# Performance work log

Measured on AMD Instinct MI355X. Metric: run time of the kernel, lower is better.

## Reference

```python
import jax, jax.numpy as jnp
import numpy as np
from math import sqrt

ALPHA = 1.0
EPS = 1e-8


def setup_inputs() -> dict:
    key = jax.random.key(0)
    k1, k2, k3 = jax.random.split(key, 3)
    B, L, S, H, E = 4, 2048, 2048, 8, 64
    queries = jax.random.normal(k1, (B, L, H, E), dtype=jnp.float32)
    keys = jax.random.normal(k2, (B, S, H, E), dtype=jnp.float32)
    values = jax.random.normal(k3, (B, S, H, E), dtype=jnp.float32)
    return {"queries": queries, "keys": keys, "values": values}


def reference(queries, keys, values):
    B, L, H, E = queries.shape
    scale = 1.0 / sqrt(E)
    # [B,H,L,S] dot-product scores
    dot_product = jnp.einsum('blhe,bshe->bhls', queries, keys)
    # squared norms: [B,H,L,1] and [B,H,1,S]
    queries_norm2 = jnp.sum(queries * queries, axis=-1).transpose(0, 2, 1)[..., None]
    keys_norm2 = jnp.sum(keys * keys, axis=-1).transpose(0, 2, 1)[..., None, :]
    # wedge (exterior product) norm: |q|^2|k|^2 - (q.k)^2, clamped at 0
    wedge_norm2 = jax.nn.relu(queries_norm2 * keys_norm2 - dot_product * dot_product)
    wedge_norm = jnp.sqrt(wedge_norm2 + EPS)
    scores = ((1.0 - ALPHA) * dot_product + ALPHA * wedge_norm) * scale
    A = jax.nn.softmax(scores, axis=-1)  # dropout p=0 (eval)
    V = jnp.einsum('bhls,bshd->blhd', A, values)
    return V, jnp.mean(jnp.abs(scores))
```

## Files before the change

kernel.cpp:

```cpp
#include <hip/hip_runtime.h>
#include <hip/hip_bf16.h>


#define B_ 4
#define L_ 2048
#define S_ 2048
#define H_ 8
#define E_ 64
#define EPS_ 1e-8f
#define SC2_ 0.18033688011112042f
#define LN2_ 0.6931471805599453f
#define ROWSTR (H_ * E_)
#define NOUT ((size_t)B_ * L_ * H_ * E_)

#define K_OFF 0
#define V_OFF 8388608
#define KN_OFF 16777216
#define WS_NEED 17039360

typedef __attribute__((ext_vector_type(8))) short bf16x8;
typedef __attribute__((ext_vector_type(4))) float f32x4;
typedef __attribute__((ext_vector_type(2))) float f32x2;

union bfr8 { bf16x8 v; unsigned u[4]; };

static __device__ __forceinline__ unsigned pk2(float lo, float hi) {
  union { __hip_bfloat162 h2; unsigned u; } cv;
  cv.h2 = __float22bfloat162_rn(float2{lo, hi});
  return cv.u;
}
static __device__ __forceinline__ unsigned cvtpk(float lo, float hi) {
  unsigned r;
  asm("v_cvt_pk_bf16_f32 %0, %1, %2" : "=v"(r) : "v"(lo), "v"(hi));
  return r;
}
static __device__ __forceinline__ float fast_sqrt(float x) {
  float r; asm("v_sqrt_f32 %0, %1" : "=v"(r) : "v"(x)); return r;
}
static __device__ __forceinline__ float fast_exp2(float x) {
  float r; asm("v_exp_f32 %0, %1" : "=v"(r) : "v"(x)); return r;
}
static __device__ __forceinline__ void gload16(const void* g, void* l) {
  __builtin_amdgcn_global_load_lds((const __attribute__((address_space(1))) void*)g,
                                   (__attribute__((address_space(3))) void*)l, 16, 0, 0);
}

__global__ void prep_kv(const float* __restrict__ K, const float* __restrict__ V,
                        short* __restrict__ Kg, short* __restrict__ Vg,
                        float* __restrict__ kn2g, float* __restrict__ out) {
  const int tid = threadIdx.x;
  const int bidx = blockIdx.x;
  if (bidx == 0 && tid == 0) out[NOUT] = 0.f;
  const int st = bidx & 31;
  const int bh = bidx >> 5;
  const int b = bh >> 3, h = bh & 7;
  const size_t src_base = (size_t)b * (L_ * ROWSTR) + (size_t)(st * 64) * ROWSTR + (size_t)h * E_;

  {
    short* dst = Kg + (size_t)bidx * 4096;
    const int s = tid >> 2;
    float part = 0.f;
#pragma unroll
    for (int q = 0; q < 2; ++q) {
      const int ch = (2 * tid + q) & 7;
      const int esrc = (ch ^ (s & 7)) * 8;
      const float* sp = K + src_base + (size_t)s * ROWSTR + esrc;
      const float4 a = *reinterpret_cast<const float4*>(sp);
      const float4 c4 = *reinterpret_cast<const float4*>(sp + 4);
      part += a.x*a.x + a.y*a.y + a.z*a.z + a.w*a.w
            + c4.x*c4.x + c4.y*c4.y + c4.z*c4.z + c4.w*c4.w;
      bfr8 o;
      o.u[0] = pk2(a.x, a.y);  o.u[1] = pk2(a.z, a.w);
      o.u[2] = pk2(c4.x, c4.y); o.u[3] = pk2(c4.z, c4.w);
      *reinterpret_cast<bf16x8*>(dst + s * 64 + ch * 8) = o.v;
    }
    part += __shfl_xor(part, 1);
    part += __shfl_xor(part, 2);
    if ((tid & 3) == 0) kn2g[(size_t)bidx * 64 + s] = part;
  }

  {
    short* dst = Vg + (size_t)bidx * 4096;
    const int e = tid & 63;
    const int sc0 = tid >> 6;
#pragma unroll
    for (int q = 0; q < 2; ++q) {
      const int sc = sc0 + q * 4;
      const float* sp = V + src_base + (size_t)(sc * 8) * ROWSTR + e;
      const float v0 = sp[0];
      const float v1 = sp[1 * ROWSTR];
      const float v2 = sp[2 * ROWSTR];
      const float v3 = sp[3 * ROWSTR];
      const float v4 = sp[4 * ROWSTR];
      const float v5 = sp[5 * ROWSTR];
      const float v6 = sp[6 * ROWSTR];
      const float v7 = sp[7 * ROWSTR];
      bfr8 o;
      o.u[0] = pk2(v0, v1); o.u[1] = pk2(v2, v3);
      o.u[2] = pk2(v4, v5); o.u[3] = pk2(v6, v7);
      *reinterpret_cast<bf16x8*>(dst + e * 64 + ((sc ^ (e & 7)) * 8)) = o.v;
    }
  }
}

__launch_bounds__(256, 4)
__global__ void geom_attn(const float* __restrict__ Q,
                          const short* __restrict__ Kg,
                          const short* __restrict__ Vg,
                          const float* __restrict__ kn2g,
                          float* __restrict__ out) {
  __shared__ __align__(16) short Kl[2][4096];
  __shared__ __align__(16) short Vl[2][4096];
  __shared__ __align__(16) short Plds[4][1024];

  const int tid = threadIdx.x;
  const int lane = tid & 63;
  const int w = tid >> 6;
  const int g = lane >> 4;
  const int c = lane & 15;
  const int cx = c & 7;

  const int vbk = ((blockIdx.x & 7) << 7) + (blockIdx.x >> 3);
  const int qt = vbk & 31;
  const int bh = vbk >> 5;
  const int b = bh >> 3, h = bh & 7;
  const int q0 = qt * 64;

  const size_t qbase = (size_t)b * (L_ * ROWSTR) + (size_t)h * E_;

  bfr8 qa[2];
  float qn2sc;
  {
    const int qrow = q0 + w * 16 + c;
    const float* qp = Q + qbase + (size_t)qrow * ROWSTR;
    float qs = 0.f;
#pragma unroll
    for (int ch = 0; ch < 2; ++ch) {
      const float4 a = *reinterpret_cast<const float4*>(qp + ch * 32 + g * 8);
      const float4 b4 = *reinterpret_cast<const float4*>(qp + ch * 32 + g * 8 + 4);
      qa[ch].u[0] = pk2(a.x, a.y);  qa[ch].u[1] = pk2(a.z, a.w);
      qa[ch].u[2] = pk2(b4.x, b4.y); qa[ch].u[3] = pk2(b4.z, b4.w);
      qs += a.x*a.x + a.y*a.y + a.z*a.z + a.w*a.w
          + b4.x*b4.x + b4.y*b4.y + b4.z*b4.z + b4.w*b4.w;
    }
    qs += __shfl_xor(qs, 16);
    qs += __shfl_xor(qs, 32);
    qn2sc = qs;
  }
  const f32x2 qn2v = {qn2sc, qn2sc};
  const f32x2 eps2 = {EPS_, EPS_};
  const f32x2 sc2v = {SC2_, SC2_};

  f32x2 lsA = {0.f, 0.f}, lsB = {0.f, 0.f};
  f32x2 ssA = {0.f, 0.f}, ssB = {0.f, 0.f};
  f32x4 o[4];
#pragma unroll
  for (int dt = 0; dt < 4; ++dt) o[dt] = (f32x4){0.f, 0.f, 0.f, 0.f};

  const char* Ksrc = (const char*)(Kg + (size_t)(bh * 32) * 4096);
  const char* Vsrc = (const char*)(Vg + (size_t)(bh * 32) * 4096);
  const float* knb = kn2g + (size_t)(bh * 32) * 64;

  const int wb = w * 2048;

  f32x4 kn_cur[4], kn_nx[4];
#pragma unroll
  for (int sub = 0; sub < 4; ++sub)
    kn_cur[sub] = *reinterpret_cast<const f32x4*>(knb + sub * 16 + g * 4);

  gload16(Ksrc + wb + lane * 16,        (char*)&Kl[0][0] + wb);
  gload16(Ksrc + wb + 1024 + lane * 16, (char*)&Kl[0][0] + wb + 1024);
  gload16(Vsrc + wb + lane * 16,        (char*)&Vl[0][0] + wb);
  gload16(Vsrc + wb + 1024 + lane * 16, (char*)&Vl[0][0] + wb + 1024);

  for (int kt = 0; kt < 32; ++kt) {
    const int cb = kt & 1;
    const int nx = (kt + 1) & 31;
    __syncthreads();

#pragma unroll
    for (int sub = 0; sub < 4; ++sub)
      kn_nx[sub] = *reinterpret_cast<const f32x4*>(knb + nx * 64 + sub * 16 + g * 4);
    const char* vs = Vsrc + (size_t)nx * 8192;
    gload16(vs + wb + lane * 16,        (char*)&Vl[cb ^ 1][0] + wb);
    gload16(vs + wb + 1024 + lane * 16, (char*)&Vl[cb ^ 1][0] + wb + 1024);
    const char* ks = Ksrc + (size_t)nx * 8192;
    gload16(ks + wb + lane * 16,        (char*)&Kl[cb ^ 1][0] + wb);
    gload16(ks + wb + 1024 + lane * 16, (char*)&Kl[cb ^ 1][0] + wb + 1024);
    __builtin_amdgcn_sched_barrier(0);

#pragma unroll
    for (int sub = 0; sub < 4; ++sub) {
      f32x4 acc = (f32x4){0.f, 0.f, 0.f, 0.f};
#pragma unroll
      for (int ch = 0; ch < 2; ++ch) {
        const int idx = (sub * 16 + c) * 64 + (((ch * 4 + g) ^ cx) << 3);
        const bf16x8 kh8 = *reinterpret_cast<const bf16x8*>(&Kl[cb][idx]);
        acc = __builtin_amdgcn_mfma_f32_16x16x32_bf16(kh8, qa[ch].v, acc, 0, 0, 0);
      }
      const f32x2 d0 = {acc[0], acc[1]};
      const f32x2 d1 = {acc[2], acc[3]};
      const f32x2 ka = {kn_cur[sub][0], kn_cur[sub][1]};
      const f32x2 kb = {kn_cur[sub][2], kn_cur[sub][3]};
      f32x2 w0 = -d0 * d0 + (qn2v * ka + eps2);
      f32x2 w1 = -d1 * d1 + (qn2v * kb + eps2);
      w0[0] = fmaxf(w0[0], EPS_); w0[1] = fmaxf(w0[1], EPS_);
      w1[0] = fmaxf(w1[0], EPS_); w1[1] = fmaxf(w1[1], EPS_);
      f32x2 s0 = {fast_sqrt(w0[0]), fast_sqrt(w0[1])};
      f32x2 s1 = {fast_sqrt(w1[0]), fast_sqrt(w1[1])};
      s0 *= sc2v; s1 *= sc2v;
      ssA += s0; ssB += s1;
      const f32x2 p0 = {fast_exp2(s0[0]), fast_exp2(s0[1])};
      const f32x2 p1 = {fast_exp2(s1[0]), fast_exp2(s1[1])};
      lsA += p0; lsB += p1;
      uint2 pw;
      pw.x = cvtpk(p0[0], p0[1]);
      pw.y = cvtpk(p1[0], p1[1]);
      const int po = c * 64 + ((sub * 16 + g * 4) ^ (cx << 3));
      *reinterpret_cast<uint2*>(&Plds[w][po]) = pw;
    }

    __builtin_amdgcn_s_setprio(1);
#pragma unroll
    for (int ks2 = 0; ks2 < 2; ++ks2) {
      const int pr = c * 64 + ((ks2 * 32 + g * 8) ^ (cx << 3));
      const bf16x8 pa = *reinterpret_cast<const bf16x8*>(&Plds[w][pr]);
#pragma unroll
      for (int dt = 0; dt < 4; ++dt) {
        const int idx = (dt * 16 + c) * 64 + (((ks2 * 4 + g) ^ cx) << 3);
        const bf16x8 vb8 = *reinterpret_cast<const bf16x8*>(&Vl[cb][idx]);
        o[dt] = __builtin_amdgcn_mfma_f32_16x16x32_bf16(pa, vb8, o[dt], 0, 0, 0);
      }
    }
    __builtin_amdgcn_s_setprio(0);
#pragma unroll
    for (int sub = 0; sub < 4; ++sub) kn_cur[sub] = kn_nx[sub];
  }

  const f32x2 lsT = lsA + lsB;
  float lsum = lsT[0] + lsT[1];
  lsum += __shfl_xor(lsum, 16);
  lsum += __shfl_xor(lsum, 32);
  const float rinv = 1.0f / lsum;

#pragma unroll
  for (int i = 0; i < 4; ++i) {
    const float inv = __shfl(rinv, g * 4 + i);
    const int qrow = q0 + w * 16 + g * 4 + i;
    float* op = out + (size_t)b * (L_ * ROWSTR) + (size_t)qrow * ROWSTR + (size_t)h * E_;
#pragma unroll
    for (int dt = 0; dt < 4; ++dt)
      op[dt * 16 + c] = o[dt][i] * inv;
  }

  const f32x2 ssT = ssA + ssB;
  float ssum = ssT[0] + ssT[1];
#pragma unroll
  for (int m = 1; m < 64; m <<= 1) ssum += __shfl_xor(ssum, m);
  if (lane == 0) atomicAdd(out + NOUT, ssum * (LN2_ / 134217728.0f));
}

extern "C" void kernel_launch(void* const* d_in, const int* in_sizes, int n_in,
                              void* d_out, int out_size, void* d_ws, size_t ws_size,
                              hipStream_t stream) {
  const float* Q = (const float*)d_in[0];
  const float* K = (const float*)d_in[1];
  const float* V = (const float*)d_in[2];
  float* out = (float*)d_out;

  short* Kg = (short*)((char*)d_ws + K_OFF);
  short* Vg = (short*)((char*)d_ws + V_OFF);
  float* kn2g = (float*)((char*)d_ws + KN_OFF);

  prep_kv<<<dim3(1024), dim3(256), 0, stream>>>(K, V, Kg, Vg, kn2g, out);
  geom_attn<<<dim3(1024), dim3(256), 0, stream>>>(Q, Kg, Vg, kn2g, out);
}
```

Measured before the change: 189.4 us.

## Load K/V fragments directly from global memory instead of LDS double buffer

Removes the shared-memory double-buffered K/V staging (global_load_lds, __syncthreads, prefetch of next tile and key norms). Each wave instead reads its K and V MFMA fragments straight from global memory, relying on L1/L2 caching since all four waves read the same tile. This drops block-wide barriers and LDS traffic, and the lower LDS use may allow more occupancy. In exchange, global reads are no longer overlapped with compute through explicit prefetching, and each wave issues its own redundant global loads.

```diff
diff --git a/kernel.cpp b/kernel.cpp
--- a/kernel.cpp
+++ b/kernel.cpp
@@ -16,7 +16,6 @@
 #define K_OFF 0
 #define V_OFF 8388608
 #define KN_OFF 16777216
-#define WS_NEED 17039360
 
 typedef __attribute__((ext_vector_type(8))) short bf16x8;
 typedef __attribute__((ext_vector_type(4))) float f32x4;
@@ -39,10 +38,6 @@
 }
 static __device__ __forceinline__ float fast_exp2(float x) {
   float r; asm("v_exp_f32 %0, %1" : "=v"(r) : "v"(x)); return r;
-}
-static __device__ __forceinline__ void gload16(const void* g, void* l) {
-  __builtin_amdgcn_global_load_lds((const __attribute__((address_space(1))) void*)g,
-                                   (__attribute__((address_space(3))) void*)l, 16, 0, 0);
 }
 
 __global__ void prep_kv(const float* __restrict__ K, const float* __restrict__ V,
@@ -109,30 +104,27 @@
                           const short* __restrict__ Vg,
                           const float* __restrict__ kn2g,
                           float* __restrict__ out) {
-  __shared__ __align__(16) short Kl[2][4096];
-  __shared__ __align__(16) short Vl[2][4096];
   __shared__ __align__(16) short Plds[4][1024];
 
   const int tid = threadIdx.x;
   const int lane = tid & 63;
   const int w = tid >> 6;
+  const int c = lane & 15;
   const int g = lane >> 4;
-  const int c = lane & 15;
   const int cx = c & 7;
 
   const int vbk = ((blockIdx.x & 7) << 7) + (blockIdx.x >> 3);
-  const int qt = vbk & 31;
+  const int qq = vbk & 31;
   const int bh = vbk >> 5;
   const int b = bh >> 3, h = bh & 7;
-  const int q0 = qt * 64;
+  const int q0 = qq * 64 + w * 16;
 
   const size_t qbase = (size_t)b * (L_ * ROWSTR) + (size_t)h * E_;
 
   bfr8 qa[2];
   float qn2sc;
   {
-    const int qrow = q0 + w * 16 + c;
-    const float* qp = Q + qbase + (size_t)qrow * ROWSTR;
+    const float* qp = Q + qbase + (size_t)(q0 + c) * ROWSTR;
     float qs = 0.f;
 #pragma unroll
     for (int ch = 0; ch < 2; ++ch) {
@@ -157,51 +149,36 @@
 #pragma unroll
   for (int dt = 0; dt < 4; ++dt) o[dt] = (f32x4){0.f, 0.f, 0.f, 0.f};
 
-  const char* Ksrc = (const char*)(Kg + (size_t)(bh * 32) * 4096);
-  const char* Vsrc = (const char*)(Vg + (size_t)(bh * 32) * 4096);
+  const short* Ktile = Kg + (size_t)(bh * 32) * 4096;
+  const short* Vtile = Vg + (size_t)(bh * 32) * 4096;
   const float* knb = kn2g + (size_t)(bh * 32) * 64;
 
-  const int wb = w * 2048;
-
-  f32x4 kn_cur[4], kn_nx[4];
-#pragma unroll
-  for (int sub = 0; sub < 4; ++sub)
-    kn_cur[sub] = *reinterpret_cast<const f32x4*>(knb + sub * 16 + g * 4);
-
-  gload16(Ksrc + wb + lane * 16,        (char*)&Kl[0][0] + wb);
-  gload16(Ksrc + wb + 1024 + lane * 16, (char*)&Kl[0][0] + wb + 1024);
-  gload16(Vsrc + wb + lane * 16,        (char*)&Vl[0][0] + wb);
-  gload16(Vsrc + wb + 1024 + lane * 16, (char*)&Vl[0][0] + wb + 1024);
-
   for (int kt = 0; kt < 32; ++kt) {
-    const int cb = kt & 1;
-    const int nx = (kt + 1) & 31;
-    __syncthreads();
-
+    const short* Kt = Ktile + (size_t)kt * 4096;
+    const short* Vt = Vtile + (size_t)kt * 4096;
+
+    f32x4 kn[4];
 #pragma unroll
     for (int sub = 0; sub < 4; ++sub)
-      kn_nx[sub] = *reinterpret_cast<const f32x4*>(knb + nx * 64 + sub * 16 + g * 4);
-    const char* vs = Vsrc + (size_t)nx * 8192;
-    gload16(vs + wb + lane * 16,        (char*)&Vl[cb ^ 1][0] + wb);
-    gload16(vs + wb + 1024 + lane * 16, (char*)&Vl[cb ^ 1][0] + wb + 1024);
-    const char* ks = Ksrc + (size_t)nx * 8192;
-    gload16(ks + wb + lane * 16,        (char*)&Kl[cb ^ 1][0] + wb);
-    gload16(ks + wb + 1024 + lane * 16, (char*)&Kl[cb ^ 1][0] + wb + 1024);
-    __builtin_amdgcn_sched_barrier(0);
+      kn[sub] = *reinterpret_cast<const f32x4*>(knb + kt * 64 + sub * 16 + g * 4);
+
+    bf16x8 kf[8];
+#pragma unroll
+    for (int sub = 0; sub < 4; ++sub)
+#pragma unroll
+      for (int ch = 0; ch < 2; ++ch)
+        kf[sub * 2 + ch] = *reinterpret_cast<const bf16x8*>(
+            Kt + (sub * 16 + c) * 64 + (((ch * 4 + g) ^ cx) << 3));
 
 #pragma unroll
     for (int sub = 0; sub < 4; ++sub) {
       f32x4 acc = (f32x4){0.f, 0.f, 0.f, 0.f};
-#pragma unroll
-      for (int ch = 0; ch < 2; ++ch) {
-        const int idx = (sub * 16 + c) * 64 + (((ch * 4 + g) ^ cx) << 3);
-        const bf16x8 kh8 = *reinterpret_cast<const bf16x8*>(&Kl[cb][idx]);
-        acc = __builtin_amdgcn_mfma_f32_16x16x32_bf16(kh8, qa[ch].v, acc, 0, 0, 0);
-      }
+      acc = __builtin_amdgcn_mfma_f32_16x16x32_bf16(kf[sub * 2 + 0], qa[0].v, acc, 0, 0, 0);
+      acc = __builtin_amdgcn_mfma_f32_16x16x32_bf16(kf[sub * 2 + 1], qa[1].v, acc, 0, 0, 0);
       const f32x2 d0 = {acc[0], acc[1]};
       const f32x2 d1 = {acc[2], acc[3]};
-      const f32x2 ka = {kn_cur[sub][0], kn_cur[sub][1]};
-      const f32x2 kb = {kn_cur[sub][2], kn_cur[sub][3]};
+      const f32x2 ka = {kn[sub][0], kn[sub][1]};
+      const f32x2 kb = {kn[sub][2], kn[sub][3]};
       f32x2 w0 = -d0 * d0 + (qn2v * ka + eps2);
       f32x2 w1 = -d1 * d1 + (qn2v * kb + eps2);
       w0[0] = fmaxf(w0[0], EPS_); w0[1] = fmaxf(w0[1], EPS_);
@@ -220,21 +197,19 @@
       *reinterpret_cast<uint2*>(&Plds[w][po]) = pw;
     }
 
-    __builtin_amdgcn_s_setprio(1);
 #pragma unroll
     for (int ks2 = 0; ks2 < 2; ++ks2) {
+      bf16x8 vf[4];
+#pragma unroll
+      for (int dt = 0; dt < 4; ++dt)
+        vf[dt] = *reinterpret_cast<const bf16x8*>(
+            Vt + (dt * 16 + c) * 64 + (((ks2 * 4 + g) ^ cx) << 3));
       const int pr = c * 64 + ((ks2 * 32 + g * 8) ^ (cx << 3));
       const bf16x8 pa = *reinterpret_cast<const bf16x8*>(&Plds[w][pr]);
 #pragma unroll
-      for (int dt = 0; dt < 4; ++dt) {
-        const int idx = (dt * 16 + c) * 64 + (((ks2 * 4 + g) ^ cx) << 3);
-        const bf16x8 vb8 = *reinterpret_cast<const bf16x8*>(&Vl[cb][idx]);
-        o[dt] = __builtin_amdgcn_mfma_f32_16x16x32_bf16(pa, vb8, o[dt], 0, 0, 0);
-      }
-    }
-    __builtin_amdgcn_s_setprio(0);
-#pragma unroll
-    for (int sub = 0; sub < 4; ++sub) kn_cur[sub] = kn_nx[sub];
+      for (int dt = 0; dt < 4; ++dt)
+        o[dt] = __builtin_amdgcn_mfma_f32_16x16x32_bf16(pa, vf[dt], o[dt], 0, 0, 0);
+    }
   }
 
   const f32x2 lsT = lsA + lsB;
@@ -246,7 +221,7 @@
 #pragma unroll
   for (int i = 0; i < 4; ++i) {
     const float inv = __shfl(rinv, g * 4 + i);
-    const int qrow = q0 + w * 16 + g * 4 + i;
+    const int qrow = q0 + g * 4 + i;
     float* op = out + (size_t)b * (L_ * ROWSTR) + (size_t)qrow * ROWSTR + (size_t)h * E_;
 #pragma unroll
     for (int dt = 0; dt < 4; ++dt)
```

New measurement: 244.1 us. 28.8% more time.

## Convert K to bf16 in natural layout and apply swizzle at LDS load time

Applied to the files above, without the earlier changes.

The K preprocessing now does a flat, fully coalesced fp32-to-bf16 conversion in extra blocks, keeping the original [B,L,H,E] layout. The norm pass reads K separately. The attention kernel gathers 16-byte chunks per row with the XOR swizzle applied on the global side. The V swizzle moves from the prep kernel to the load addresses as well. The prep write becomes cheaper, but the attention kernel's K loads are now strided by row, which may reduce load efficiency.

```diff
diff --git a/kernel.cpp b/kernel.cpp
--- a/kernel.cpp
+++ b/kernel.cpp
@@ -16,7 +16,6 @@
 #define K_OFF 0
 #define V_OFF 8388608
 #define KN_OFF 16777216
-#define WS_NEED 17039360
 
 typedef __attribute__((ext_vector_type(8))) short bf16x8;
 typedef __attribute__((ext_vector_type(4))) float f32x4;
@@ -51,32 +50,41 @@
   const int tid = threadIdx.x;
   const int bidx = blockIdx.x;
   if (bidx == 0 && tid == 0) out[NOUT] = 0.f;
+
+  if (bidx >= 1024) {
+    const int kidx = bidx - 1024;
+    const size_t base = (size_t)kidx * 4096 + (size_t)tid * 8;
+#pragma unroll
+    for (int it = 0; it < 2; ++it) {
+      const size_t idx = base + (size_t)it * 2048;
+      const float4 a = *reinterpret_cast<const float4*>(K + idx);
+      const float4 c4 = *reinterpret_cast<const float4*>(K + idx + 4);
+      bfr8 o;
+      o.u[0] = pk2(a.x, a.y);  o.u[1] = pk2(a.z, a.w);
+      o.u[2] = pk2(c4.x, c4.y); o.u[3] = pk2(c4.z, c4.w);
+      *reinterpret_cast<bf16x8*>(Kg + idx) = o.v;
+    }
+    return;
+  }
+
   const int st = bidx & 31;
   const int bh = bidx >> 5;
   const int b = bh >> 3, h = bh & 7;
   const size_t src_base = (size_t)b * (L_ * ROWSTR) + (size_t)(st * 64) * ROWSTR + (size_t)h * E_;
 
   {
-    short* dst = Kg + (size_t)bidx * 4096;
     const int s = tid >> 2;
+    const int f = tid & 3;
+    const float* sp = K + src_base + (size_t)s * ROWSTR;
     float part = 0.f;
 #pragma unroll
-    for (int q = 0; q < 2; ++q) {
-      const int ch = (2 * tid + q) & 7;
-      const int esrc = (ch ^ (s & 7)) * 8;
-      const float* sp = K + src_base + (size_t)s * ROWSTR + esrc;
-      const float4 a = *reinterpret_cast<const float4*>(sp);
-      const float4 c4 = *reinterpret_cast<const float4*>(sp + 4);
-      part += a.x*a.x + a.y*a.y + a.z*a.z + a.w*a.w
-            + c4.x*c4.x + c4.y*c4.y + c4.z*c4.z + c4.w*c4.w;
-      bfr8 o;
-      o.u[0] = pk2(a.x, a.y);  o.u[1] = pk2(a.z, a.w);
-      o.u[2] = pk2(c4.x, c4.y); o.u[3] = pk2(c4.z, c4.w);
-      *reinterpret_cast<bf16x8*>(dst + s * 64 + ch * 8) = o.v;
+    for (int j = 0; j < 4; ++j) {
+      const float4 a = *reinterpret_cast<const float4*>(sp + f * 4 + j * 16);
+      part += a.x*a.x + a.y*a.y + a.z*a.z + a.w*a.w;
     }
     part += __shfl_xor(part, 1);
     part += __shfl_xor(part, 2);
-    if ((tid & 3) == 0) kn2g[(size_t)bidx * 64 + s] = part;
+    if (f == 0) kn2g[(size_t)bidx * 64 + s] = part;
   }
 
   {
@@ -98,7 +106,7 @@
       bfr8 o;
       o.u[0] = pk2(v0, v1); o.u[1] = pk2(v2, v3);
       o.u[2] = pk2(v4, v5); o.u[3] = pk2(v6, v7);
-      *reinterpret_cast<bf16x8*>(dst + e * 64 + ((sc ^ (e & 7)) * 8)) = o.v;
+      *reinterpret_cast<bf16x8*>(dst + e * 64 + sc * 8) = o.v;
     }
   }
 }
@@ -157,10 +165,18 @@
 #pragma unroll
   for (int dt = 0; dt < 4; ++dt) o[dt] = (f32x4){0.f, 0.f, 0.f, 0.f};
 
-  const char* Ksrc = (const char*)(Kg + (size_t)(bh * 32) * 4096);
-  const char* Vsrc = (const char*)(Vg + (size_t)(bh * 32) * 4096);
+  const int lr = lane >> 3;
+  const int lch = lane & 7;
+  const int kr1 = w * 16 + lr;
+  const int kr2 = kr1 + 8;
+  const short* Kbh = Kg + (size_t)b * (L_ * ROWSTR) + (size_t)h * E_;
+  const short* ks1 = Kbh + (size_t)(q0 * 0 + kr1) * ROWSTR + ((lch ^ (kr1 & 7)) << 3);
+  const short* ks2 = Kbh + (size_t)kr2 * ROWSTR + ((lch ^ (kr2 & 7)) << 3);
+  const short* Vbh = Vg + (size_t)bh * (32 * 4096);
+  const short* vs1 = Vbh + (size_t)kr1 * 64 + ((lch ^ (kr1 & 7)) << 3);
+  const short* vs2 = Vbh + (size_t)kr2 * 64 + ((lch ^ (kr2 & 7)) << 3);
+
   const float* knb = kn2g + (size_t)(bh * 32) * 64;
-
   const int wb = w * 2048;
 
   f32x4 kn_cur[4], kn_nx[4];
@@ -168,10 +184,10 @@
   for (int sub = 0; sub < 4; ++sub)
     kn_cur[sub] = *reinterpret_cast<const f32x4*>(knb + sub * 16 + g * 4);
 
-  gload16(Ksrc + wb + lane * 16,        (char*)&Kl[0][0] + wb);
-  gload16(Ksrc + wb + 1024 + lane * 16, (char*)&Kl[0][0] + wb + 1024);
-  gload16(Vsrc + wb + lane * 16,        (char*)&Vl[0][0] + wb);
-  gload16(Vsrc + wb + 1024 + lane * 16, (char*)&Vl[0][0] + wb + 1024);
+  gload16(ks1, (char*)&Kl[0][0] + wb + lane * 16);
+  gload16(ks2, (char*)&Kl[0][0] + wb + 1024 + lane * 16);
+  gload16(vs1, (char*)&Vl[0][0] + wb + lane * 16);
+  gload16(vs2, (char*)&Vl[0][0] + wb + 1024 + lane * 16);
 
   for (int kt = 0; kt < 32; ++kt) {
     const int cb = kt & 1;
@@ -181,12 +197,10 @@
 #pragma unroll
     for (int sub = 0; sub < 4; ++sub)
       kn_nx[sub] = *reinterpret_cast<const f32x4*>(knb + nx * 64 + sub * 16 + g * 4);
-    const char* vs = Vsrc + (size_t)nx * 8192;
-    gload16(vs + wb + lane * 16,        (char*)&Vl[cb ^ 1][0] + wb);
-    gload16(vs + wb + 1024 + lane * 16, (char*)&Vl[cb ^ 1][0] + wb + 1024);
-    const char* ks = Ksrc + (size_t)nx * 8192;
-    gload16(ks + wb + lane * 16,        (char*)&Kl[cb ^ 1][0] + wb);
-    gload16(ks + wb + 1024 + lane * 16, (char*)&Kl[cb ^ 1][0] + wb + 1024);
+    gload16(vs1 + (size_t)nx * 4096, (char*)&Vl[cb ^ 1][0] + wb + lane * 16);
+    gload16(vs2 + (size_t)nx * 4096, (char*)&Vl[cb ^ 1][0] + wb + 1024 + lane * 16);
+    gload16(ks1 + (size_t)nx * (64 * ROWSTR), (char*)&Kl[cb ^ 1][0] + wb + lane * 16);
+    gload16(ks2 + (size_t)nx * (64 * ROWSTR), (char*)&Kl[cb ^ 1][0] + wb + 1024 + lane * 16);
     __builtin_amdgcn_sched_barrier(0);
 
 #pragma unroll
@@ -222,12 +236,12 @@
 
     __builtin_amdgcn_s_setprio(1);
 #pragma unroll
-    for (int ks2 = 0; ks2 < 2; ++ks2) {
-      const int pr = c * 64 + ((ks2 * 32 + g * 8) ^ (cx << 3));
+    for (int ks2i = 0; ks2i < 2; ++ks2i) {
+      const int pr = c * 64 + ((ks2i * 32 + g * 8) ^ (cx << 3));
       const bf16x8 pa = *reinterpret_cast<const bf16x8*>(&Plds[w][pr]);
 #pragma unroll
       for (int dt = 0; dt < 4; ++dt) {
-        const int idx = (dt * 16 + c) * 64 + (((ks2 * 4 + g) ^ cx) << 3);
+        const int idx = (dt * 16 + c) * 64 + (((ks2i * 4 + g) ^ cx) << 3);
         const bf16x8 vb8 = *reinterpret_cast<const bf16x8*>(&Vl[cb][idx]);
         o[dt] = __builtin_amdgcn_mfma_f32_16x16x32_bf16(pa, vb8, o[dt], 0, 0, 0);
       }
@@ -272,6 +286,6 @@
   short* Vg = (short*)((char*)d_ws + V_OFF);
   float* kn2g = (float*)((char*)d_ws + KN_OFF);
 
-  prep_kv<<<dim3(1024), dim3(256), 0, stream>>>(K, V, Kg, Vg, kn2g, out);
+  prep_kv<<<dim3(2048), dim3(256), 0, stream>>>(K, V, Kg, Vg, kn2g, out);
   geom_attn<<<dim3(1024), dim3(256), 0, stream>>>(Q, Kg, Vg, kn2g, out);
 }
```

After: 197.5 us. +4.3%, slower.
